# Performance work log

Measured on AMD Instinct MI355X. Metric: run time of the kernel, lower is better.

## Reference

```python
import jax, jax.numpy as jnp
import numpy as np
import math

N, S, E, BS = 8, 8192, 256, 8


def setup_inputs() -> dict:
    key = jax.random.key(0)
    k1, k2, k3 = jax.random.split(key, 3)
    seq_vector = jax.random.normal(k1, (N, S, E), dtype=jnp.float32)
    # Conv1d weight [target_dim, source_dim] (kernel size 1 squeezed), default torch init scale
    bound = 1.0 / math.sqrt(E)
    W = jax.random.uniform(k2, (E, E), minval=-bound, maxval=bound, dtype=jnp.float32)
    sigma = math.sqrt(1.0 / (BS * E))
    bias = jax.random.uniform(k3, (BS,), minval=-sigma, maxval=sigma, dtype=jnp.float32)
    return {"seq_vector": seq_vector, "W": W, "bias": bias}


def reference(seq_vector, W, bias):
    n, s, e = seq_vector.shape
    bs = bias.shape[0]
    # 1x1 conv == per-token projection: [N,S,E] x [T,E] -> [N,S,T]
    features = jnp.einsum('nse,te->nst', seq_vector, W)
    # group sequence into blocks: [N, S//bs, bs, T]
    fb = features.reshape(n, s // bs, bs, -1)
    # blockwise causal (strictly lower-triangular) sum == exclusive cumsum over block dim
    excl = jnp.cumsum(fb, axis=2) - fb
    # position i gets bias[i]; position 0 additionally gets bias[0] a second time
    b_eff = bias.at[0].add(bias[0])  # [bs]
    out = excl + b_eff[None, None, :, None]
    return out.reshape(n, s, -1)
```

## Files before the change

kernel.cpp:

```cpp
#include <hip/hip_runtime.h>


typedef short short8 __attribute__((ext_vector_type(8)));
typedef float floatx4 __attribute__((ext_vector_type(4)));
typedef unsigned short ushort4v __attribute__((ext_vector_type(4)));

typedef const __attribute__((address_space(1))) unsigned int* gas_u32p;
typedef __attribute__((address_space(3))) unsigned int* las_u32p;

#define WAIT_VMCNT(n) __builtin_amdgcn_s_waitcnt(0x0F70 | ((n) & 0xF) | ((((n) >> 4) & 0x3) << 14))

__device__ __forceinline__ void gl2lds16(const void* g, void* l) {
    __builtin_amdgcn_global_load_lds((gas_u32p)g, (las_u32p)l, 16, 0, 0);
}

__device__ __forceinline__ unsigned short f2bf(float f) {
    union { float f; unsigned int u; } v;
    v.f = f;
    unsigned int u = v.u + 0x7fffu + ((v.u >> 16) & 1u);
    return (unsigned short)(u >> 16);
}

__device__ __forceinline__ short8 pack8(float4 f0, float4 f1) {
    short8 r;
    r[0] = (short)f2bf(f0.x); r[1] = (short)f2bf(f0.y);
    r[2] = (short)f2bf(f0.z); r[3] = (short)f2bf(f0.w);
    r[4] = (short)f2bf(f1.x); r[5] = (short)f2bf(f1.y);
    r[6] = (short)f2bf(f1.z); r[7] = (short)f2bf(f1.w);
    return r;
}

__global__ __launch_bounds__(256) void wconv_kernel(
    const float* __restrict__ W, unsigned short* __restrict__ Wb)
{
    const int i = (blockIdx.x * 256 + threadIdx.x) * 4;
    float4 f = *(const float4*)(W + i);
    ushort4v v;
    v[0] = f2bf(f.x); v[1] = f2bf(f.y); v[2] = f2bf(f.z); v[3] = f2bf(f.w);
    *(ushort4v*)(Wb + i) = v;
}

__global__ __launch_bounds__(256, 2) void bcl_gemm_kernel(
    const float* __restrict__ X, const unsigned short* __restrict__ Wb,
    const float* __restrict__ bias, float* __restrict__ out)
{
    __shared__ float buf[3][128 * 32];
    __shared__ unsigned short bW[64 * 256];

    const int tid  = threadIdx.x;
    const int lane = tid & 63;
    const int w    = tid >> 6;
    const int bx   = blockIdx.x;
    const int mg   = bx >> 2;
    const int ng   = bx & 3;

    const int cl = lane & 15;
    const int q  = lane >> 4;

    const int srow = lane >> 3;
    const int sseg = (lane & 7) ^ srow;
    const float* gsrc0 = X + (size_t)(mg * 128 + w * 32 + srow) * 256 + sseg * 4;

#define STAGE(c, b)                                                            \
    do {                                                                       \
        const float* _g = gsrc0 + (c) * 32;                                    \
        _Pragma("unroll")                                                      \
        for (int _j = 0; _j < 4; ++_j)                                         \
            gl2lds16(_g + _j * 8 * 256, &buf[b][(w * 32 + _j * 8) * 32]);      \
    } while (0)

    {
        #pragma unroll
        for (int j = 0; j < 8; ++j) {
            const int n    = j * 8 + w * 2 + (lane >> 5);
            const int seg  = lane & 31;
            const int lseg = seg ^ (n & 15);
            const unsigned short* g =
                Wb + (size_t)(ng * 64 + n) * 256 + lseg * 8;
            gl2lds16(g, &bW[(size_t)(j * 256 + w * 64) * 8]);
        }
    }

    STAGE(0, 0);
    STAGE(1, 1);
    WAIT_VMCNT(8);
    __syncthreads();

    floatx4 acc[2][4];
    #pragma unroll
    for (int mt = 0; mt < 2; ++mt)
        #pragma unroll
        for (int nt = 0; nt < 4; ++nt)
            acc[mt][nt] = (floatx4){0.f, 0.f, 0.f, 0.f};

#define KSTEP(c, ALLOW)                                                        \
    do {                                                                       \
        if ((c) + 2 < 8) STAGE((c) + 2, ((c) + 2) % 3);                        \
        __builtin_amdgcn_sched_barrier(0);                                     \
        WAIT_VMCNT(ALLOW);                                                     \
        __builtin_amdgcn_sched_barrier(0);                                     \
        short8 Bf[4];                                                          \
        _Pragma("unroll")                                                      \
        for (int nt = 0; nt < 4; ++nt)                                         \
            Bf[nt] = *(const short8*)                                          \
                &bW[(nt * 16 + cl) * 256 + ((((c) * 4 + q) ^ cl) * 8)];        \
        float4 af[2][2];                                                       \
        _Pragma("unroll")                                                      \
        for (int mt = 0; mt < 2; ++mt)                                         \
            _Pragma("unroll")                                                  \
            for (int h = 0; h < 2; ++h)                                        \
                af[mt][h] = *(const float4*)                                   \
                    &buf[(c) % 3][(w * 32 + mt * 16 + cl) * 32 +               \
                                  ((((q << 1) | h) ^ (cl & 7)) << 2)];         \
        short8 a0 = pack8(af[0][0], af[0][1]);                                 \
        short8 a1 = pack8(af[1][0], af[1][1]);                                 \
        _Pragma("unroll")                                                      \
        for (int nt = 0; nt < 4; ++nt) {                                       \
            acc[0][nt] = __builtin_amdgcn_mfma_f32_16x16x32_bf16(              \
                a0, Bf[nt], acc[0][nt], 0, 0, 0);                              \
            acc[1][nt] = __builtin_amdgcn_mfma_f32_16x16x32_bf16(              \
                a1, Bf[nt], acc[1][nt], 0, 0, 0);                              \
        }                                                                      \
    } while (0)

    KSTEP(0, 8);
    KSTEP(1, 8);
    KSTEP(2, 8);
    KSTEP(3, 8);
    KSTEP(4, 8);
    KSTEP(5, 8);
    KSTEP(6, 4);
    KSTEP(7, 0);
#undef KSTEP

    float be[4];
    {
        const int off = (q & 1) * 4;
        be[0] = bias[off + 0];
        be[1] = bias[off + 1];
        be[2] = bias[off + 2];
        be[3] = bias[off + 3];
        if (off == 0) be[0] += bias[0];
    }

    float* epi = &buf[0][w * 32 * 32];

    #pragma unroll
    for (int p = 0; p < 4; ++p) {
        const int mt = p >> 1;
        const bool act = ((q >> 1) == (p & 1));
        #pragma unroll
        for (int nt = 0; nt < 4; ++nt) {
            floatx4 v = acc[mt][nt];
            float p1 = v[0];
            float p2 = p1 + v[1];
            float p3 = p2 + v[2];
            float tot = p3 + v[3];
            float below = __shfl_up(tot, 16);
            float p0 = 0.f;
            if (q & 1) { p0 = below; p1 += below; p2 += below; p3 += below; }
            if (act) {
                float* dst = epi + (q & 1) * 4 * 64 + nt * 16 + cl;
                dst[0]   = p0 + be[0];
                dst[64]  = p1 + be[1];
                dst[128] = p2 + be[2];
                dst[192] = p3 + be[3];
            }
        }
        #pragma unroll
        for (int k = 0; k < 2; ++k) {
            const int r   = k * 4 + (lane >> 4);
            const int c16 = lane & 15;
            floatx4 vv = *(const floatx4*)&epi[r * 64 + c16 * 4];
            const size_t grow = (size_t)(mg * 128 + w * 32 + p * 8 + r);
            *(floatx4*)&out[grow * 256 + ng * 64 + c16 * 4] = vv;
        }
    }
#undef STAGE
}

extern "C" void kernel_launch(void* const* d_in, const int* in_sizes, int n_in,
                              void* d_out, int out_size, void* d_ws, size_t ws_size,
                              hipStream_t stream)
{
    const float* X = (const float*)d_in[0];
    const float* W = (const float*)d_in[1];
    const float* B = (const float*)d_in[2];
    float* out = (float*)d_out;
    unsigned short* Wb = (unsigned short*)d_ws;

    wconv_kernel<<<dim3(64), dim3(256), 0, stream>>>(W, Wb);
    bcl_gemm_kernel<<<dim3(2048), dim3(256), 0, stream>>>(X, Wb, B, out);
}
```

Baseline: 148.1 us.

## Use 8 waves per block with 16-row warp tiles and XCD-aware block mapping

Doubles the block to 512 threads so each wave computes a 16x64 output tile instead of 32x64, halving per-wave accumulators and staging work, with loads, wait counts and the epilogue adjusted to match. Block indices are also remapped so each XCD handles a contiguous range of row groups, which should improve L2 locality for the four column blocks that share the same X rows. The intent is more waves in flight to hide memory latency on a bandwidth-bound GEMM with a prefix-sum epilogue. In exchange, each B fragment loaded from LDS now feeds half as many MFMAs, and the epilogue writes to two staging buffers.

```diff
diff --git a/kernel.cpp b/kernel.cpp
--- a/kernel.cpp
+++ b/kernel.cpp
@@ -40,7 +40,7 @@
     *(ushort4v*)(Wb + i) = v;
 }
 
-__global__ __launch_bounds__(256, 2) void bcl_gemm_kernel(
+__global__ __launch_bounds__(512, 4) void bcl_gemm_kernel(
     const float* __restrict__ X, const unsigned short* __restrict__ Wb,
     const float* __restrict__ bias, float* __restrict__ out)
 {
@@ -51,47 +51,48 @@
     const int lane = tid & 63;
     const int w    = tid >> 6;
     const int bx   = blockIdx.x;
-    const int mg   = bx >> 2;
-    const int ng   = bx & 3;
+
+    const int xcd = bx & 7;
+    const int u   = bx >> 3;
+    const int mg  = xcd * 64 + (u >> 2);
+    const int ng  = u & 3;
 
     const int cl = lane & 15;
     const int q  = lane >> 4;
 
     const int srow = lane >> 3;
     const int sseg = (lane & 7) ^ srow;
-    const float* gsrc0 = X + (size_t)(mg * 128 + w * 32 + srow) * 256 + sseg * 4;
+    const float* gsrc0 = X + (size_t)(mg * 128 + w * 16 + srow) * 256 + sseg * 4;
 
 #define STAGE(c, b)                                                            \
     do {                                                                       \
         const float* _g = gsrc0 + (c) * 32;                                    \
         _Pragma("unroll")                                                      \
-        for (int _j = 0; _j < 4; ++_j)                                         \
-            gl2lds16(_g + _j * 8 * 256, &buf[b][(w * 32 + _j * 8) * 32]);      \
+        for (int _j = 0; _j < 2; ++_j)                                         \
+            gl2lds16(_g + _j * 8 * 256, &buf[b][(w * 16 + _j * 8) * 32]);      \
     } while (0)
 
     {
         #pragma unroll
-        for (int j = 0; j < 8; ++j) {
-            const int n    = j * 8 + w * 2 + (lane >> 5);
-            const int seg  = lane & 31;
+        for (int j = 0; j < 4; ++j) {
+            const int n    = j * 16 + (tid >> 5);
+            const int seg  = tid & 31;
             const int lseg = seg ^ (n & 15);
             const unsigned short* g =
                 Wb + (size_t)(ng * 64 + n) * 256 + lseg * 8;
-            gl2lds16(g, &bW[(size_t)(j * 256 + w * 64) * 8]);
+            gl2lds16(g, &bW[(size_t)(j * 512 + w * 64) * 8]);
         }
     }
 
     STAGE(0, 0);
     STAGE(1, 1);
-    WAIT_VMCNT(8);
+    WAIT_VMCNT(4);
     __syncthreads();
 
-    floatx4 acc[2][4];
+    floatx4 acc[4];
     #pragma unroll
-    for (int mt = 0; mt < 2; ++mt)
-        #pragma unroll
-        for (int nt = 0; nt < 4; ++nt)
-            acc[mt][nt] = (floatx4){0.f, 0.f, 0.f, 0.f};
+    for (int nt = 0; nt < 4; ++nt)
+        acc[nt] = (floatx4){0.f, 0.f, 0.f, 0.f};
 
 #define KSTEP(c, ALLOW)                                                        \
     do {                                                                       \
@@ -104,32 +105,26 @@
         for (int nt = 0; nt < 4; ++nt)                                         \
             Bf[nt] = *(const short8*)                                          \
                 &bW[(nt * 16 + cl) * 256 + ((((c) * 4 + q) ^ cl) * 8)];        \
-        float4 af[2][2];                                                       \
+        float4 af[2];                                                          \
         _Pragma("unroll")                                                      \
-        for (int mt = 0; mt < 2; ++mt)                                         \
-            _Pragma("unroll")                                                  \
-            for (int h = 0; h < 2; ++h)                                        \
-                af[mt][h] = *(const float4*)                                   \
-                    &buf[(c) % 3][(w * 32 + mt * 16 + cl) * 32 +               \
-                                  ((((q << 1) | h) ^ (cl & 7)) << 2)];         \
-        short8 a0 = pack8(af[0][0], af[0][1]);                                 \
-        short8 a1 = pack8(af[1][0], af[1][1]);                                 \
+        for (int h = 0; h < 2; ++h)                                            \
+            af[h] = *(const float4*)                                           \
+                &buf[(c) % 3][(w * 16 + cl) * 32 +                             \
+                              ((((q << 1) | h) ^ (cl & 7)) << 2)];             \
+        short8 a0 = pack8(af[0], af[1]);                                       \
         _Pragma("unroll")                                                      \
-        for (int nt = 0; nt < 4; ++nt) {                                       \
-            acc[0][nt] = __builtin_amdgcn_mfma_f32_16x16x32_bf16(              \
-                a0, Bf[nt], acc[0][nt], 0, 0, 0);                              \
-            acc[1][nt] = __builtin_amdgcn_mfma_f32_16x16x32_bf16(              \
-                a1, Bf[nt], acc[1][nt], 0, 0, 0);                              \
-        }                                                                      \
+        for (int nt = 0; nt < 4; ++nt)                                         \
+            acc[nt] = __builtin_amdgcn_mfma_f32_16x16x32_bf16(                 \
+                a0, Bf[nt], acc[nt], 0, 0, 0);                                 \
     } while (0)
 
-    KSTEP(0, 8);
-    KSTEP(1, 8);
-    KSTEP(2, 8);
-    KSTEP(3, 8);
-    KSTEP(4, 8);
-    KSTEP(5, 8);
-    KSTEP(6, 4);
+    KSTEP(0, 4);
+    KSTEP(1, 4);
+    KSTEP(2, 4);
+    KSTEP(3, 4);
+    KSTEP(4, 4);
+    KSTEP(5, 4);
+    KSTEP(6, 2);
     KSTEP(7, 0);
 #undef KSTEP
 
@@ -143,15 +138,16 @@
         if (off == 0) be[0] += bias[0];
     }
 
-    float* epi = &buf[0][w * 32 * 32];
+    float* epi0 = &buf[0][(w * 16) * 32];
+    float* epi1 = &buf[1][(w * 16) * 32];
 
     #pragma unroll
-    for (int p = 0; p < 4; ++p) {
-        const int mt = p >> 1;
-        const bool act = ((q >> 1) == (p & 1));
+    for (int p = 0; p < 2; ++p) {
+        float* epi = p ? epi1 : epi0;
+        const bool act = ((q >> 1) == p);
         #pragma unroll
         for (int nt = 0; nt < 4; ++nt) {
-            floatx4 v = acc[mt][nt];
+            floatx4 v = acc[nt];
             float p1 = v[0];
             float p2 = p1 + v[1];
             float p3 = p2 + v[2];
@@ -172,7 +168,7 @@
             const int r   = k * 4 + (lane >> 4);
             const int c16 = lane & 15;
             floatx4 vv = *(const floatx4*)&epi[r * 64 + c16 * 4];
-            const size_t grow = (size_t)(mg * 128 + w * 32 + p * 8 + r);
+            const size_t grow = (size_t)(mg * 128 + w * 16 + p * 8 + r);
             *(floatx4*)&out[grow * 256 + ng * 64 + c16 * 4] = vv;
         }
     }
@@ -190,5 +186,5 @@
     unsigned short* Wb = (unsigned short*)d_ws;
 
     wconv_kernel<<<dim3(64), dim3(256), 0, stream>>>(W, Wb);
-    bcl_gemm_kernel<<<dim3(2048), dim3(256), 0, stream>>>(X, Wb, B, out);
+    bcl_gemm_kernel<<<dim3(2048), dim3(512), 0, stream>>>(X, Wb, B, out);
 }
```

Measured after the change: 141.4 us. 4.5% less time.
